# Performance work log

Measured on AMD Instinct MI355X. Metric: run time of the kernel, lower is better.

## Reference

```python
import jax, jax.numpy as jnp
import numpy as np

EMBED_DIM = 1024
NUM_HEADS = 16
HEAD_DIM = EMBED_DIM // NUM_HEADS


def setup_inputs() -> dict:
    key = jax.random.key(0)
    k_x, k_wqkv, k_bqkv, k_wout, k_bout = jax.random.split(key, 5)
    s = 1.0 / np.sqrt(EMBED_DIM)
    return {
        "x": jax.random.normal(k_x, (2, 2048, EMBED_DIM), dtype=jnp.float32),
        "w_qkv": jax.random.uniform(k_wqkv, (EMBED_DIM, 3 * EMBED_DIM), jnp.float32, -s, s),
        "b_qkv": jax.random.uniform(k_bqkv, (3 * EMBED_DIM,), jnp.float32, -s, s),
        "w_out": jax.random.uniform(k_wout, (EMBED_DIM, EMBED_DIM), jnp.float32, -s, s),
        "b_out": jax.random.uniform(k_bout, (EMBED_DIM,), jnp.float32, -s, s),
    }


def reference(x, w_qkv, b_qkv, w_out, b_out):
    B, S, D = x.shape
    H, Hd = NUM_HEADS, HEAD_DIM
    # qkv projection, then per-head chunk: layout matches torch view(B,S,H,3*Hd).chunk(3,-1)
    qkv = (x @ w_qkv + b_qkv).reshape(B, S, H, 3, Hd)  # [B,S,H,3,Hd]
    q = qkv[..., 0, :]  # [B,S,H,Hd]
    k = qkv[..., 1, :]
    v = qkv[..., 2, :]
    scale = 1.0 / np.sqrt(Hd).astype(np.float32)
    scores = jnp.einsum("bqhd,bkhd->bhqk", q, k) * scale  # [B,H,S,S]
    probs = jax.nn.softmax(scores, axis=-1)
    out = jnp.einsum("bhqk,bkhd->bqhd", probs, v).reshape(B, S, D)
    return out @ w_out + b_out
```

## Files before the change

### kernel.cpp

```cpp
#include <hip/hip_runtime.h>
#include <hip/hip_bf16.h>


typedef __bf16 bf16;
typedef __bf16 bf16x8 __attribute__((ext_vector_type(8)));
typedef float  f32x4  __attribute__((ext_vector_type(4)));
typedef float  f32x16 __attribute__((ext_vector_type(16)));
typedef unsigned int uint;
typedef unsigned int uint2v __attribute__((ext_vector_type(2)));

__device__ __forceinline__ void gload_lds16(const void* g, void* l) {
  __builtin_amdgcn_global_load_lds(
      (const __attribute__((address_space(1))) unsigned int*)g,
      (__attribute__((address_space(3))) unsigned int*)l, 16, 0, 0);
}

__device__ __forceinline__ uint pkbf16(float lo, float hi) {
  union { bf16 h[2]; uint u; } t;
  t.h[0] = (bf16)lo; t.h[1] = (bf16)hi;
  return t.u;
}

__device__ __forceinline__ void pl32swapu(uint& a, uint& b) {
  uint2v r = __builtin_amdgcn_permlane32_swap(a, b, false, false);
  a = r.x; b = r.y;
}
__device__ __forceinline__ void pl32swapf(float& a, float& b) {
  uint ua = __builtin_bit_cast(uint, a), ub = __builtin_bit_cast(uint, b);
  pl32swapu(ua, ub);
  a = __builtin_bit_cast(float, ua); b = __builtin_bit_cast(float, ub);
}

__global__ __launch_bounds__(256) void k_convert(const float* __restrict__ in,
                                                 bf16* __restrict__ out, int n) {
  int i = (blockIdx.x * blockDim.x + threadIdx.x) * 8;
  if (i >= n) return;
  float4 a = *(const float4*)(in + i);
  float4 b = *(const float4*)(in + i + 4);
  bf16x8 o;
  o[0] = (bf16)a.x; o[1] = (bf16)a.y; o[2] = (bf16)a.z; o[3] = (bf16)a.w;
  o[4] = (bf16)b.x; o[5] = (bf16)b.y; o[6] = (bf16)b.z; o[7] = (bf16)b.w;
  *(bf16x8*)(out + i) = o;
}

__global__ __launch_bounds__(256) void k_transpose(const float* __restrict__ in,
                                                   bf16* __restrict__ out, int K, int N) {
  __shared__ float tile[32][33];
  int n0 = blockIdx.x * 32, k0 = blockIdx.y * 32;
  int tx = threadIdx.x, ty = threadIdx.y;
#pragma unroll
  for (int i = 0; i < 4; i++)
    tile[ty + i * 8][tx] = in[(size_t)(k0 + ty + i * 8) * N + n0 + tx];
  __syncthreads();
#pragma unroll
  for (int i = 0; i < 4; i++)
    out[(size_t)(n0 + ty + i * 8) * K + k0 + tx] = (bf16)tile[tx][ty + i * 8];
}

template<int BM, int BN>
__device__ __forceinline__ void gemm_tile(const bf16* __restrict__ A, const bf16* __restrict__ B,
                                          int K, int m0, int n0,
                                          bf16* As, bf16* Bs, f32x4 acc[BM / 32][BN / 32]) {
  const int tid  = threadIdx.x;
  const int lane = tid & 63;
  const int wr   = (tid >> 7) & 1;
  const int wc   = (tid >> 6) & 1;
  auto stage = [&](int k0, int b) {
#pragma unroll
    for (int i = 0; i < BM / 64; i++) {
      int row = i * 64 + (tid >> 2);
      int sw  = (tid & 3) ^ (row & 3);
      gload_lds16(A + (size_t)(m0 + row) * K + k0 + sw * 8, (char*)As + b * (BM * 64) + i * 4096 + tid * 16);
    }
#pragma unroll
    for (int i = 0; i < BN / 64; i++) {
      int row = i * 64 + (tid >> 2);
      int sw  = (tid & 3) ^ (row & 3);
      gload_lds16(B + (size_t)(n0 + row) * K + k0 + sw * 8, (char*)Bs + b * (BN * 64) + i * 4096 + tid * 16);
    }
  };
  stage(0, 0);
  const int nk = K / 32;
  for (int t = 0; t < nk; t++) {
    const int cur = t & 1;
    if (t + 1 < nk) {
      stage((t + 1) * 32, cur ^ 1);
      if constexpr (BM / 64 + BN / 64 == 4) asm volatile("s_waitcnt vmcnt(4)" ::: "memory");
      else                                  asm volatile("s_waitcnt vmcnt(3)" ::: "memory");
    } else {
      asm volatile("s_waitcnt vmcnt(0)" ::: "memory");
    }
    __builtin_amdgcn_s_barrier();
    asm volatile("" ::: "memory");
    bf16x8 af[BM / 32], bfr[BN / 32];
#pragma unroll
    for (int r = 0; r < BM / 32; r++) {
      int ra = wr * (BM / 2) + r * 16 + (lane & 15);
      af[r]  = *(const bf16x8*)((const char*)As + cur * (BM * 64) + ra * 64 + ((((lane >> 4) << 4)) ^ ((ra & 3) << 4)));
    }
#pragma unroll
    for (int c = 0; c < BN / 32; c++) {
      int rb = wc * (BN / 2) + c * 16 + (lane & 15);
      bfr[c] = *(const bf16x8*)((const char*)Bs + cur * (BN * 64) + rb * 64 + ((((lane >> 4) << 4)) ^ ((rb & 3) << 4)));
    }
#pragma unroll
    for (int r = 0; r < BM / 32; r++)
#pragma unroll
      for (int c = 0; c < BN / 32; c++)
        acc[r][c] = __builtin_amdgcn_mfma_f32_16x16x32_bf16(af[r], bfr[c], acc[r][c], 0, 0, 0);
    asm volatile("" ::: "memory");
    __builtin_amdgcn_s_barrier();
    asm volatile("" ::: "memory");
  }
}

__global__ __launch_bounds__(256) void k_gemm_qkv(const bf16* __restrict__ A, const bf16* __restrict__ Bt,
                                                  const float* __restrict__ bias,
                                                  bf16* __restrict__ qb, bf16* __restrict__ kb,
                                                  bf16* __restrict__ vtb) {
  __shared__ bf16 As[2 * 128 * 32];
  __shared__ bf16 Bs[2 * 128 * 32];
  int m0 = blockIdx.x * 128, n0 = blockIdx.y * 128;
  f32x4 zero = {0.f, 0.f, 0.f, 0.f};
  f32x4 acc[4][4];
#pragma unroll
  for (int r = 0; r < 4; r++)
#pragma unroll
    for (int c = 0; c < 4; c++) acc[r][c] = zero;
  gemm_tile<128, 128>(A, Bt, 1024, m0, n0, As, Bs, acc);
  const int lane = threadIdx.x & 63;
  const int wr = (threadIdx.x >> 7) & 1, wc = (threadIdx.x >> 6) & 1;
  const float QS = 0.125f * 1.4426950408889634f;
#pragma unroll
  for (int r = 0; r < 4; r++) {
    int mbase = m0 + wr * 64 + r * 16 + ((lane >> 4) << 2);
#pragma unroll
    for (int c = 0; c < 4; c++) {
      int n = n0 + wc * 64 + c * 16 + (lane & 15);
      float bv = bias[n];
      int h = n / 192, rem = n % 192;
      int sel = rem >> 6, d = rem & 63;
#pragma unroll
      for (int g = 0; g < 4; g++) {
        int m = mbase + g;
        int b_ = m >> 11, s = m & 2047;
        int bh = b_ * 16 + h;
        float v = acc[r][c][g] + bv;
        if (sel == 0)      qb[((size_t)bh * 2048 + s) * 64 + d] = (bf16)(v * QS);
        else if (sel == 1) kb[((size_t)bh * 2048 + s) * 64 + d] = (bf16)v;
        else               vtb[((size_t)bh * 64 + d) * 2048 + s] = (bf16)v;
      }
    }
  }
}

__global__ __launch_bounds__(256) void k_gemm_out(const bf16* __restrict__ A, const bf16* __restrict__ Bt,
                                                  const float* __restrict__ bias,
                                                  float* __restrict__ out) {
  __shared__ bf16 As[2 * 64 * 32];
  __shared__ bf16 Bs[2 * 128 * 32];
  int m0 = blockIdx.x * 64, n0 = blockIdx.y * 128;
  f32x4 zero = {0.f, 0.f, 0.f, 0.f};
  f32x4 acc[2][4];
#pragma unroll
  for (int r = 0; r < 2; r++)
#pragma unroll
    for (int c = 0; c < 4; c++) acc[r][c] = zero;
  gemm_tile<64, 128>(A, Bt, 1024, m0, n0, As, Bs, acc);
  const int lane = threadIdx.x & 63;
  const int wr = (threadIdx.x >> 7) & 1, wc = (threadIdx.x >> 6) & 1;
#pragma unroll
  for (int r = 0; r < 2; r++) {
    int mbase = m0 + wr * 32 + r * 16 + ((lane >> 4) << 2);
#pragma unroll
    for (int c = 0; c < 4; c++) {
      int n = n0 + wc * 64 + c * 16 + (lane & 15);
      float bv = bias[n];
#pragma unroll
      for (int g = 0; g < 4; g++)
        out[(size_t)(mbase + g) * 1024 + n] = acc[r][c][g] + bv;
    }
  }
}

__global__ __launch_bounds__(512, 4) void k_attn(const bf16* __restrict__ qb, const bf16* __restrict__ kb,
                                                 const bf16* __restrict__ vtb, bf16* __restrict__ ob) {
  __shared__ char SMEM[65536];
  const int tid  = threadIdx.x;
  const int lane = tid & 63;
  const int wave = tid >> 6;
  const int qsub = wave & 3;
  const int half = wave >> 2;
  const int ln31 = lane & 31;
  const int g    = lane >> 5;

  int l = blockIdx.x;
  int x = l & 7, j = l >> 3;
  int qt = j & 15;
  int bh = x * 4 + (j >> 4);

  const int q0 = qt * 128 + qsub * 32;

  bf16x8 qf[4];
  {
    const bf16* qp = qb + ((size_t)bh * 2048 + q0 + ln31) * 64 + g * 8;
#pragma unroll
    for (int dc = 0; dc < 4; dc++) qf[dc] = *(const bf16x8*)(qp + dc * 16);
  }

  const f32x16 z16 = 0.f;
  f32x16 O0 = 0.f, O1 = 0.f;
  float lacc[4] = {0.f, 0.f, 0.f, 0.f};

  const int r0 = tid >> 3, c0 = tid & 7;
  const int swb = (c0 ^ (r0 & 7)) * 8;
  const bf16* kg0 = kb  + ((size_t)bh * 2048 +        r0) * 64 + swb;
  const bf16* kg1 = kb  + ((size_t)bh * 2048 + 1024 + r0) * 64 + swb;
  const bf16* vg0 = vtb + ((size_t)bh * 64 + r0) * 2048 +        swb;
  const bf16* vg1 = vtb + ((size_t)bh * 64 + r0) * 2048 + 1024 + swb;
  auto stage = [&](int t, int s) {
    char* base = SMEM + s * 32768 + tid * 16;
    gload_lds16(kg0 + (size_t)t * 4096, base);
    gload_lds16(kg1 + (size_t)t * 4096, base + 8192);
    gload_lds16(vg0 + t * 64,           base + 16384);
    gload_lds16(vg1 + t * 64,           base + 24576);
  };

  const int rs = (ln31 & 7) << 4;
  bf16x8 pf[4];

  stage(0, 0);
  for (int t = 0; t < 16; t++) {
    asm volatile("s_waitcnt vmcnt(0)" ::: "memory");
    __builtin_amdgcn_s_barrier();
    asm volatile("" ::: "memory");
    if (t + 1 < 16) stage(t + 1, (t + 1) & 1);

    const char* Kc = SMEM + (t & 1) * 32768 + half * 8192;
    const char* Vc = SMEM + (t & 1) * 32768 + (2 + half) * 8192;
    const char* kr0 = Kc + ln31 * 128;
    const char* kr1 = Kc + (32 + ln31) * 128;

    f32x16 s0v, s1v;
    __builtin_amdgcn_s_setprio(1);
    {
      bf16x8 k0 = *(const bf16x8*)(kr0 + ((g << 4) ^ rs));
      bf16x8 k1 = *(const bf16x8*)(kr1 + ((g << 4) ^ rs));
      s0v = __builtin_amdgcn_mfma_f32_32x32x16_bf16(k0, qf[0], z16, 0, 0, 0);
      s1v = __builtin_amdgcn_mfma_f32_32x32x16_bf16(k1, qf[0], z16, 0, 0, 0);
    }
#pragma unroll
    for (int dc = 1; dc < 4; dc++) {
      bf16x8 ka = *(const bf16x8*)(kr0 + (((dc * 2 + g) << 4) ^ rs));
      bf16x8 kb_ = *(const bf16x8*)(kr1 + (((dc * 2 + g) << 4) ^ rs));
      s0v = __builtin_amdgcn_mfma_f32_32x32x16_bf16(ka, qf[dc], s0v, 0, 0, 0);
      s1v = __builtin_amdgcn_mfma_f32_32x32x16_bf16(kb_, qf[dc], s1v, 0, 0, 0);
    }
    __builtin_amdgcn_s_setprio(0);

#pragma unroll
    for (int r = 0; r < 16; r++) {
      s0v[r] = __builtin_amdgcn_exp2f(s0v[r]);
      s1v[r] = __builtin_amdgcn_exp2f(s1v[r]);
    }
#pragma unroll
    for (int r = 0; r < 4; r++)
      lacc[r] += ((s0v[r] + s0v[r + 4]) + (s0v[r + 8] + s0v[r + 12]))
               + ((s1v[r] + s1v[r + 4]) + (s1v[r + 8] + s1v[r + 12]));
#pragma unroll
    for (int kc = 0; kc < 4; kc++) {
      const int rb = (kc & 1) * 8;
      uint w0, w1, w2, w3;
      if (kc < 2) {
        w0 = pkbf16(s0v[rb + 0], s0v[rb + 1]); w1 = pkbf16(s0v[rb + 2], s0v[rb + 3]);
        w2 = pkbf16(s0v[rb + 4], s0v[rb + 5]); w3 = pkbf16(s0v[rb + 6], s0v[rb + 7]);
      } else {
        w0 = pkbf16(s1v[rb + 0], s1v[rb + 1]); w1 = pkbf16(s1v[rb + 2], s1v[rb + 3]);
        w2 = pkbf16(s1v[rb + 4], s1v[rb + 5]); w3 = pkbf16(s1v[rb + 6], s1v[rb + 7]);
      }
      pl32swapu(w0, w2);
      pl32swapu(w1, w3);
      union { uint w[4]; bf16x8 v; } pu;
      pu.w[0] = w0; pu.w[1] = w1; pu.w[2] = w2; pu.w[3] = w3;
      pf[kc] = pu.v;
    }

    __builtin_amdgcn_s_setprio(1);
#pragma unroll
    for (int kc = 0; kc < 4; kc++) {
      bf16x8 vf0 = *(const bf16x8*)(Vc + ln31 * 128 + (((kc * 2 + g) << 4) ^ rs));
      bf16x8 vf1 = *(const bf16x8*)(Vc + (32 + ln31) * 128 + (((kc * 2 + g) << 4) ^ rs));
      O0 = __builtin_amdgcn_mfma_f32_32x32x16_bf16(vf0, pf[kc], O0, 0, 0, 0);
      O1 = __builtin_amdgcn_mfma_f32_32x32x16_bf16(vf1, pf[kc], O1, 0, 0, 0);
    }
    __builtin_amdgcn_s_setprio(0);
    asm volatile("" ::: "memory");
  }

  float l_r = (lacc[0] + lacc[1]) + (lacc[2] + lacc[3]);
  { float o = l_r; pl32swapf(l_r, o); l_r += o; }

  float* Opart = (float*)SMEM;
  float* Ls    = (float*)(SMEM + 36864);
  __syncthreads();
  if (half == 1) {
    float* my = Opart + (qsub * 64 + lane) * 36;
#pragma unroll
    for (int c = 0; c < 4; c++) {
      f32x4 a = {O0[c * 4], O0[c * 4 + 1], O0[c * 4 + 2], O0[c * 4 + 3]};
      f32x4 b = {O1[c * 4], O1[c * 4 + 1], O1[c * 4 + 2], O1[c * 4 + 3]};
      *(f32x4*)(my + c * 4) = a;
      *(f32x4*)(my + 16 + c * 4) = b;
    }
    if (lane < 32) Ls[qsub * 32 + ln31] = l_r;
  }
  __syncthreads();
  bf16 (*Os)[32][72] = reinterpret_cast<bf16 (*)[32][72]>(SMEM + 40960);
  if (half == 0) {
    const float* pr = Opart + (qsub * 64 + lane) * 36;
#pragma unroll
    for (int c = 0; c < 4; c++) {
      f32x4 a = *(const f32x4*)(pr + c * 4);
      f32x4 b = *(const f32x4*)(pr + 16 + c * 4);
#pragma unroll
      for (int k = 0; k < 4; k++) { O0[c * 4 + k] += a[k]; O1[c * 4 + k] += b[k]; }
    }
    l_r += Ls[qsub * 32 + ln31];
    float inv = 1.0f / l_r;
#pragma unroll
    for (int r = 0; r < 16; r++) {
      int d0 = (r & 3) + 8 * (r >> 2) + 4 * g;
      Os[qsub][ln31][d0]      = (bf16)(O0[r] * inv);
      Os[qsub][ln31][d0 + 32] = (bf16)(O1[r] * inv);
    }
  }
  __syncthreads();
  if (half == 0) {
    int b_ = bh >> 4, h = bh & 15;
#pragma unroll
    for (int it = 0; it < 4; it++) {
      int cid = it * 64 + lane;
      int row = cid >> 3, c = cid & 7;
      bf16x8 v8o = *(const bf16x8*)&Os[qsub][row][c * 8];
      *(bf16x8*)(ob + ((size_t)(b_ * 2048 + q0 + row)) * 1024 + h * 64 + c * 8) = v8o;
    }
  }
}

extern "C" void kernel_launch(void* const* d_in, const int* in_sizes, int n_in,
                              void* d_out, int out_size, void* d_ws, size_t ws_size,
                              hipStream_t stream) {
  const float* x     = (const float*)d_in[0];
  const float* w_qkv = (const float*)d_in[1];
  const float* b_qkv = (const float*)d_in[2];
  const float* w_out = (const float*)d_in[3];
  const float* b_out = (const float*)d_in[4];
  float* out = (float*)d_out;

  char* ws = (char*)d_ws;
  bf16* xb  = (bf16*)ws;
  bf16* wqT = (bf16*)(ws + (8ull  << 20));
  bf16* woT = (bf16*)(ws + (14ull << 20));
  bf16* qb  = (bf16*)(ws + (16ull << 20));
  bf16* kb  = (bf16*)(ws + (24ull << 20));
  bf16* vtb = (bf16*)(ws + (32ull << 20));

  k_convert<<<2048, 256, 0, stream>>>(x, xb, 4194304);
  k_transpose<<<dim3(96, 32), dim3(32, 8), 0, stream>>>(w_qkv, wqT, 1024, 3072);
  k_transpose<<<dim3(32, 32), dim3(32, 8), 0, stream>>>(w_out, woT, 1024, 1024);
  k_gemm_qkv<<<dim3(32, 24), 256, 0, stream>>>(xb, wqT, b_qkv, qb, kb, vtb);
  k_attn<<<512, 512, 0, stream>>>(qb, kb, vtb, xb);
  k_gemm_out<<<dim3(64, 8), 256, 0, stream>>>(xb, woT, b_out, out);
}
```

Measured before the change: 125.2 us.

## Permute QKV weight rows for coalesced epilogue and software-pipeline attention loop

The QKV weight transpose now permutes output rows so that each 128-column GEMM tile covers only Q, only K, or only V across two heads. The epilogue stages results in LDS and writes coalesced 16-byte vectors, including a transposed write for V, replacing the earlier scattered scalar bf16 stores. The attention loop is software-pipelined so that QK^T for tile t is issued together with PV for tile t-1, and the exp/softmax runs after the next stage load is issued. This adds an extra barrier per iteration and LDS round trips in the GEMM epilogue.

```diff
diff --git a/kernel.cpp b/kernel.cpp
--- a/kernel.cpp
+++ b/kernel.cpp
@@ -43,6 +43,7 @@
   *(bf16x8*)(out + i) = o;
 }
 
+template<bool PERM>
 __global__ __launch_bounds__(256) void k_transpose(const float* __restrict__ in,
                                                    bf16* __restrict__ out, int K, int N) {
   __shared__ float tile[32][33];
@@ -53,8 +54,15 @@
     tile[ty + i * 8][tx] = in[(size_t)(k0 + ty + i * 8) * N + n0 + tx];
   __syncthreads();
 #pragma unroll
-  for (int i = 0; i < 4; i++)
-    out[(size_t)(n0 + ty + i * 8) * K + k0 + tx] = (bf16)tile[tx][ty + i * 8];
+  for (int i = 0; i < 4; i++) {
+    int n = n0 + ty + i * 8;
+    int row = n;
+    if (PERM) {
+      int rem = n % 192;
+      row = (rem >> 6) * 1024 + (n / 192) * 64 + (rem & 63);
+    }
+    out[(size_t)row * K + k0 + tx] = (bf16)tile[tx][ty + i * 8];
+  }
 }
 
 template<int BM, int BN>
@@ -118,8 +126,9 @@
                                                   const float* __restrict__ bias,
                                                   bf16* __restrict__ qb, bf16* __restrict__ kb,
                                                   bf16* __restrict__ vtb) {
-  __shared__ bf16 As[2 * 128 * 32];
-  __shared__ bf16 Bs[2 * 128 * 32];
+  __shared__ char GS[32768];
+  bf16* As = (bf16*)GS;
+  bf16* Bs = (bf16*)(GS + 16384);
   int m0 = blockIdx.x * 128, n0 = blockIdx.y * 128;
   f32x4 zero = {0.f, 0.f, 0.f, 0.f};
   f32x4 acc[4][4];
@@ -128,28 +137,54 @@
 #pragma unroll
     for (int c = 0; c < 4; c++) acc[r][c] = zero;
   gemm_tile<128, 128>(A, Bt, 1024, m0, n0, As, Bs, acc);
-  const int lane = threadIdx.x & 63;
-  const int wr = (threadIdx.x >> 7) & 1, wc = (threadIdx.x >> 6) & 1;
-  const float QS = 0.125f * 1.4426950408889634f;
+
+  const int tid  = threadIdx.x;
+  const int lane = tid & 63;
+  const int wr = (tid >> 7) & 1, wc = (tid >> 6) & 1;
+  const int group = n0 >> 10;
+  const int hb = (n0 & 1023) >> 6;
+  const int b_ = m0 >> 11;
+  const float QSs = 0.125f * 1.4426950408889634f;
+
+  __syncthreads();
+  char* TL = GS;
 #pragma unroll
   for (int r = 0; r < 4; r++) {
-    int mbase = m0 + wr * 64 + r * 16 + ((lane >> 4) << 2);
+    int mloc = wr * 64 + r * 16 + ((lane >> 4) << 2);
 #pragma unroll
     for (int c = 0; c < 4; c++) {
-      int n = n0 + wc * 64 + c * 16 + (lane & 15);
-      float bv = bias[n];
-      int h = n / 192, rem = n % 192;
-      int sel = rem >> 6, d = rem & 63;
+      int nloc = wc * 64 + c * 16 + (lane & 15);
+      int np = n0 + nloc;
+      float bv = bias[((np & 1023) >> 6) * 192 + group * 64 + (np & 63)];
 #pragma unroll
       for (int g = 0; g < 4; g++) {
-        int m = mbase + g;
-        int b_ = m >> 11, s = m & 2047;
-        int bh = b_ * 16 + h;
         float v = acc[r][c][g] + bv;
-        if (sel == 0)      qb[((size_t)bh * 2048 + s) * 64 + d] = (bf16)(v * QS);
-        else if (sel == 1) kb[((size_t)bh * 2048 + s) * 64 + d] = (bf16)v;
-        else               vtb[((size_t)bh * 64 + d) * 2048 + s] = (bf16)v;
+        if (group == 0) v *= QSs;
+        int row = (group < 2) ? (mloc + g) : nloc;
+        int col = (group < 2) ? nloc : (mloc + g);
+        *(bf16*)(TL + row * 256 + col * 2) = (bf16)v;
       }
+    }
+  }
+  __syncthreads();
+  if (group < 2) {
+    bf16* dst = (group == 0) ? qb : kb;
+#pragma unroll
+    for (int it = 0; it < 8; it++) {
+      int cid = it * 256 + tid;
+      int sl = cid >> 4, sub = cid & 15;
+      int hh = hb + (sub >> 3), ck = sub & 7;
+      bf16x8 v8 = *(const bf16x8*)(TL + sl * 256 + (sub << 4));
+      *(bf16x8*)(dst + ((size_t)(b_ * 16 + hh) * 2048 + (m0 & 2047) + sl) * 64 + ck * 8) = v8;
+    }
+  } else {
+#pragma unroll
+    for (int it = 0; it < 8; it++) {
+      int cid = it * 256 + tid;
+      int row = cid >> 4, ck = cid & 15;
+      int hh = hb + (row >> 6), dd = row & 63;
+      bf16x8 v8 = *(const bf16x8*)(TL + row * 256 + (ck << 4));
+      *(bf16x8*)(vtb + ((size_t)(b_ * 16 + hh) * 64 + dd) * 2048 + (m0 & 2047) + ck * 8) = v8;
     }
   }
 }
@@ -211,6 +246,7 @@
   const f32x16 z16 = 0.f;
   f32x16 O0 = 0.f, O1 = 0.f;
   float lacc[4] = {0.f, 0.f, 0.f, 0.f};
+  bf16x8 pf[4];
 
   const int r0 = tid >> 3, c0 = tid & 7;
   const int swb = (c0 ^ (r0 & 7)) * 8;
@@ -227,22 +263,10 @@
   };
 
   const int rs = (ln31 & 7) << 4;
-  bf16x8 pf[4];
-
-  stage(0, 0);
-  for (int t = 0; t < 16; t++) {
-    asm volatile("s_waitcnt vmcnt(0)" ::: "memory");
-    __builtin_amdgcn_s_barrier();
-    asm volatile("" ::: "memory");
-    if (t + 1 < 16) stage(t + 1, (t + 1) & 1);
-
-    const char* Kc = SMEM + (t & 1) * 32768 + half * 8192;
-    const char* Vc = SMEM + (t & 1) * 32768 + (2 + half) * 8192;
+
+  auto qk = [&](const char* Kc, f32x16& s0v, f32x16& s1v) {
     const char* kr0 = Kc + ln31 * 128;
     const char* kr1 = Kc + (32 + ln31) * 128;
-
-    f32x16 s0v, s1v;
-    __builtin_amdgcn_s_setprio(1);
     {
       bf16x8 k0 = *(const bf16x8*)(kr0 + ((g << 4) ^ rs));
       bf16x8 k1 = *(const bf16x8*)(kr1 + ((g << 4) ^ rs));
@@ -256,8 +280,19 @@
       s0v = __builtin_amdgcn_mfma_f32_32x32x16_bf16(ka, qf[dc], s0v, 0, 0, 0);
       s1v = __builtin_amdgcn_mfma_f32_32x32x16_bf16(kb_, qf[dc], s1v, 0, 0, 0);
     }
-    __builtin_amdgcn_s_setprio(0);
-
+  };
+
+  auto pv = [&](const char* Vc) {
+#pragma unroll
+    for (int kc = 0; kc < 4; kc++) {
+      bf16x8 vf0 = *(const bf16x8*)(Vc + ln31 * 128 + (((kc * 2 + g) << 4) ^ rs));
+      bf16x8 vf1 = *(const bf16x8*)(Vc + (32 + ln31) * 128 + (((kc * 2 + g) << 4) ^ rs));
+      O0 = __builtin_amdgcn_mfma_f32_32x32x16_bf16(vf0, pf[kc], O0, 0, 0, 0);
+      O1 = __builtin_amdgcn_mfma_f32_32x32x16_bf16(vf1, pf[kc], O1, 0, 0, 0);
+    }
+  };
+
+  auto softmax = [&](f32x16& s0v, f32x16& s1v) {
 #pragma unroll
     for (int r = 0; r < 16; r++) {
       s0v[r] = __builtin_amdgcn_exp2f(s0v[r]);
@@ -284,18 +319,35 @@
       pu.w[0] = w0; pu.w[1] = w1; pu.w[2] = w2; pu.w[3] = w3;
       pf[kc] = pu.v;
     }
-
+  };
+
+  stage(0, 0);
+  asm volatile("s_waitcnt vmcnt(0)" ::: "memory");
+  __builtin_amdgcn_s_barrier();
+  asm volatile("" ::: "memory");
+  stage(1, 1);
+  f32x16 sA, sB;
+  qk(SMEM + half * 8192, sA, sB);
+  softmax(sA, sB);
+
+  for (int t = 1; t < 16; t++) {
+    asm volatile("s_waitcnt vmcnt(0)" ::: "memory");
+    __builtin_amdgcn_s_barrier();
+    asm volatile("" ::: "memory");
+    const char* Kc = SMEM + (t & 1) * 32768 + half * 8192;
+    const char* Vp = SMEM + ((t - 1) & 1) * 32768 + (2 + half) * 8192;
     __builtin_amdgcn_s_setprio(1);
-#pragma unroll
-    for (int kc = 0; kc < 4; kc++) {
-      bf16x8 vf0 = *(const bf16x8*)(Vc + ln31 * 128 + (((kc * 2 + g) << 4) ^ rs));
-      bf16x8 vf1 = *(const bf16x8*)(Vc + (32 + ln31) * 128 + (((kc * 2 + g) << 4) ^ rs));
-      O0 = __builtin_amdgcn_mfma_f32_32x32x16_bf16(vf0, pf[kc], O0, 0, 0, 0);
-      O1 = __builtin_amdgcn_mfma_f32_32x32x16_bf16(vf1, pf[kc], O1, 0, 0, 0);
-    }
+    qk(Kc, sA, sB);
+    pv(Vp);
     __builtin_amdgcn_s_setprio(0);
     asm volatile("" ::: "memory");
-  }
+    __builtin_amdgcn_s_barrier();
+    asm volatile("" ::: "memory");
+    if (t + 1 < 16) stage(t + 1, (t + 1) & 1);
+    softmax(sA, sB);
+    asm volatile("" ::: "memory");
+  }
+  pv(SMEM + 32768 + (2 + half) * 8192);
 
   float l_r = (lacc[0] + lacc[1]) + (lacc[2] + lacc[3]);
   { float o = l_r; pl32swapf(l_r, o); l_r += o; }
@@ -366,8 +418,8 @@
   bf16* vtb = (bf16*)(ws + (32ull << 20));
 
   k_convert<<<2048, 256, 0, stream>>>(x, xb, 4194304);
-  k_transpose<<<dim3(96, 32), dim3(32, 8), 0, stream>>>(w_qkv, wqT, 1024, 3072);
-  k_transpose<<<dim3(32, 32), dim3(32, 8), 0, stream>>>(w_out, woT, 1024, 1024);
+  k_transpose<true><<<dim3(96, 32), dim3(32, 8), 0, stream>>>(w_qkv, wqT, 1024, 3072);
+  k_transpose<false><<<dim3(32, 32), dim3(32, 8), 0, stream>>>(w_out, woT, 1024, 1024);
   k_gemm_qkv<<<dim3(32, 24), 256, 0, stream>>>(xb, wqT, b_qkv, qb, kb, vtb);
   k_attn<<<512, 512, 0, stream>>>(qb, kb, vtb, xb);
   k_gemm_out<<<dim3(64, 8), 256, 0, stream>>>(xb, woT, b_out, out);
```

Measured after the change: 123.7 us. Within noise of the previous version (-1.1%).
